# Performance work log

Hardware: AMD Instinct MI355X
Metric: run time of the kernel (lower is better)

Reference implementation:

```python
import jax, jax.numpy as jnp
import numpy as np

SCALE_VALUE = 4096.0


def setup_inputs() -> dict:
    key = jax.random.key(0)
    kq, kv, kk = jax.random.split(key, 3)
    B, N = 16, 4096
    return {
        "query": jax.random.normal(kq, (B, N), dtype=jnp.float32),
        "value": jax.random.normal(kv, (B, N), dtype=jnp.float32),
        "key": jax.random.normal(kk, (B, N), dtype=jnp.float32),
    }


def reference(query, value, key):
    # q,k,v: [B, N]; head dim is 1, so scores is an outer product per batch.
    # scores[b, i, j] = q[b, i] * k[b, j] / sqrt(scale)
    scores = jnp.einsum("bi,bj->bij", query, key) / jnp.sqrt(jnp.float32(SCALE_VALUE))
    distribution = jax.nn.softmax(scores, axis=-1)  # [B, N, N]
    # output[b, i] = sum_j dist[b, i, j] * v[b, j]
    output = jnp.einsum("bij,bj->bi", distribution, value)
    return output, distribution
```

## Files before the change

### kernel.cpp

```cpp
#include <hip/hip_runtime.h>


typedef float f32x4 __attribute__((ext_vector_type(4)));

constexpr int kThreads = 256;
constexpr float kInvSqrtScale = 1.0f / 64.0f;

__device__ __forceinline__ float wave_reduce_sum(float x) {
#pragma unroll
  for (int off = 32; off > 0; off >>= 1) x += __shfl_down(x, off, 64);
  return x;
}

__global__ __launch_bounds__(kThreads) void dot_attn_row_kernel(
    const float* __restrict__ q, const float* __restrict__ k,
    const float* __restrict__ v, float* __restrict__ out,
    float* __restrict__ dist, int N) {
  const int row = blockIdx.x;
  const int b = row / N;
  const float a = q[row] * kInvSqrtScale;

  const f32x4* kb = reinterpret_cast<const f32x4*>(k) + (size_t)b * (N / 4);
  const f32x4* vb = reinterpret_cast<const f32x4*>(v) + (size_t)b * (N / 4);

  f32x4 e[4];
  float s = 0.f, pv = 0.f;
#pragma unroll
  for (int t = 0; t < 4; ++t) {
    const int idx = t * kThreads + threadIdx.x;
    const f32x4 kk = kb[idx];
    const f32x4 vv = vb[idx];
    f32x4 ee;
    ee.x = __expf(a * kk.x);
    ee.y = __expf(a * kk.y);
    ee.z = __expf(a * kk.z);
    ee.w = __expf(a * kk.w);
    e[t] = ee;
    s  += (ee.x + ee.y) + (ee.z + ee.w);
    pv += (ee.x * vv.x + ee.y * vv.y) + (ee.z * vv.z + ee.w * vv.w);
  }

  s = wave_reduce_sum(s);
  pv = wave_reduce_sum(pv);
  __shared__ float red_s[4];
  __shared__ float red_pv[4];
  const int lane = threadIdx.x & 63;
  const int wid = threadIdx.x >> 6;
  if (lane == 0) { red_s[wid] = s; red_pv[wid] = pv; }
  __syncthreads();
  const float stot = (red_s[0] + red_s[1]) + (red_s[2] + red_s[3]);
  const float rinv = 1.0f / stot;

  f32x4* drow = reinterpret_cast<f32x4*>(dist) + (size_t)row * (N / 4);
#pragma unroll
  for (int t = 0; t < 4; ++t) {
    const int idx = t * kThreads + threadIdx.x;
    const f32x4 ee = e[t];
    f32x4 dd;
    dd.x = ee.x * rinv;
    dd.y = ee.y * rinv;
    dd.z = ee.z * rinv;
    dd.w = ee.w * rinv;
    __builtin_nontemporal_store(dd, &drow[idx]);
  }

  if (threadIdx.x == 0) {
    const float pvtot = (red_pv[0] + red_pv[1]) + (red_pv[2] + red_pv[3]);
    out[row] = pvtot * rinv;
  }
}

extern "C" void kernel_launch(void* const* d_in, const int* in_sizes, int n_in,
                              void* d_out, int out_size, void* d_ws, size_t ws_size,
                              hipStream_t stream) {
  const float* q = (const float*)d_in[0];
  const float* v = (const float*)d_in[1];
  const float* k = (const float*)d_in[2];

  const int S = in_sizes[0];
  const int N = (int)((size_t)out_size / S) - 1;
  float* out = (float*)d_out;
  float* dist = out + S;

  dot_attn_row_kernel<<<S, kThreads, 0, stream>>>(q, k, v, out, dist, N);
}
```

Measured before the change: 188.5 us.

## Assign one wavefront per softmax row to remove block-level reduction and barrier

Each 64-lane wavefront now processes one full row (16 float4 per lane) instead of a 256-thread block sharing a row. The row sum and the weighted sum are reduced with xor shuffles inside the wave, so the shared-memory exchange and __syncthreads are gone, and the grid shrinks fourfold. The cost is higher register use per lane (16 float4 kept live) and fewer independent blocks, which may lower occupancy. The kernel is dominated by writing the 1 GiB distribution matrix, so the gain is probably small.

Measured after the change: 195.3 us. 1.04x slower.

```diff
diff --git a/kernel.cpp b/kernel.cpp
--- a/kernel.cpp
+++ b/kernel.cpp
@@ -4,30 +4,35 @@
 typedef float f32x4 __attribute__((ext_vector_type(4)));
 
 constexpr int kThreads = 256;
+constexpr int kWavesPerBlock = kThreads / 64;
+constexpr int kIter = 16;
 constexpr float kInvSqrtScale = 1.0f / 64.0f;
 
-__device__ __forceinline__ float wave_reduce_sum(float x) {
+__device__ __forceinline__ float wave_allreduce_sum(float x) {
 #pragma unroll
-  for (int off = 32; off > 0; off >>= 1) x += __shfl_down(x, off, 64);
+  for (int m = 1; m < 64; m <<= 1) x += __shfl_xor(x, m, 64);
   return x;
 }
 
-__global__ __launch_bounds__(kThreads) void dot_attn_row_kernel(
+__global__ __launch_bounds__(kThreads) void dot_attn_wave_kernel(
     const float* __restrict__ q, const float* __restrict__ k,
     const float* __restrict__ v, float* __restrict__ out,
     float* __restrict__ dist, int N) {
-  const int row = blockIdx.x;
+  const int lane = threadIdx.x & 63;
+  const int wid = threadIdx.x >> 6;
+  const int row = blockIdx.x * kWavesPerBlock + wid;
   const int b = row / N;
   const float a = q[row] * kInvSqrtScale;
 
-  const f32x4* kb = reinterpret_cast<const f32x4*>(k) + (size_t)b * (N / 4);
-  const f32x4* vb = reinterpret_cast<const f32x4*>(v) + (size_t)b * (N / 4);
+  const int nf4 = N / 4;
+  const f32x4* kb = reinterpret_cast<const f32x4*>(k) + (size_t)b * nf4;
+  const f32x4* vb = reinterpret_cast<const f32x4*>(v) + (size_t)b * nf4;
 
-  f32x4 e[4];
+  f32x4 e[kIter];
   float s = 0.f, pv = 0.f;
 #pragma unroll
-  for (int t = 0; t < 4; ++t) {
-    const int idx = t * kThreads + threadIdx.x;
+  for (int t = 0; t < kIter; ++t) {
+    const int idx = t * 64 + lane;
     const f32x4 kk = kb[idx];
     const f32x4 vv = vb[idx];
     f32x4 ee;
@@ -40,34 +45,19 @@
     pv += (ee.x * vv.x + ee.y * vv.y) + (ee.z * vv.z + ee.w * vv.w);
   }
 
-  s = wave_reduce_sum(s);
-  pv = wave_reduce_sum(pv);
-  __shared__ float red_s[4];
-  __shared__ float red_pv[4];
-  const int lane = threadIdx.x & 63;
-  const int wid = threadIdx.x >> 6;
-  if (lane == 0) { red_s[wid] = s; red_pv[wid] = pv; }
-  __syncthreads();
-  const float stot = (red_s[0] + red_s[1]) + (red_s[2] + red_s[3]);
-  const float rinv = 1.0f / stot;
+  s = wave_allreduce_sum(s);
+  pv = wave_allreduce_sum(pv);
+  const float rinv = 1.0f / s;
 
-  f32x4* drow = reinterpret_cast<f32x4*>(dist) + (size_t)row * (N / 4);
+  f32x4* drow = reinterpret_cast<f32x4*>(dist) + (size_t)row * nf4;
 #pragma unroll
-  for (int t = 0; t < 4; ++t) {
-    const int idx = t * kThreads + threadIdx.x;
-    const f32x4 ee = e[t];
-    f32x4 dd;
-    dd.x = ee.x * rinv;
-    dd.y = ee.y * rinv;
-    dd.z = ee.z * rinv;
-    dd.w = ee.w * rinv;
+  for (int t = 0; t < kIter; ++t) {
+    const int idx = t * 64 + lane;
+    const f32x4 dd = e[t] * rinv;
     __builtin_nontemporal_store(dd, &drow[idx]);
   }
 
-  if (threadIdx.x == 0) {
-    const float pvtot = (red_pv[0] + red_pv[1]) + (red_pv[2] + red_pv[3]);
-    out[row] = pvtot * rinv;
-  }
+  if (lane == 0) out[row] = pv * rinv;
 }
 
 extern "C" void kernel_launch(void* const* d_in, const int* in_sizes, int n_in,
@@ -82,5 +72,6 @@
   float* out = (float*)d_out;
   float* dist = out + S;
 
-  dot_attn_row_kernel<<<S, kThreads, 0, stream>>>(q, k, v, out, dist, N);
+  dot_attn_wave_kernel<<<S / kWavesPerBlock, kThreads, 0, stream>>>(
+      q, k, v, out, dist, N);
 }
```
